# Optimization experiments

Measured on AMD Instinct MI355X. Metric: run time of the kernel, lower is better.

The kernel has to match this reference:

```python
import jax, jax.numpy as jnp
import numpy as np

B, T, D, H, L, O = 256, 256, 64, 512, 2, 10


def _uniform(key, shape, scale):
    return jax.random.uniform(key, shape, jnp.float32, -scale, scale)


def setup_inputs() -> dict:
    key = jax.random.key(0)
    ks = jax.random.split(key, 16)
    s = 1.0 / np.sqrt(H)  # PyTorch default init bound for RNN and Linear(H, .)
    inp = {
        "x": jax.random.normal(ks[0], (B, T, D), jnp.float32),
        # layer 0: input D -> H
        "w_ih0": _uniform(ks[1], (H, D), s),
        "w_hh0": _uniform(ks[2], (H, H), s),
        "b_ih0": _uniform(ks[3], (H,), s),
        "b_hh0": _uniform(ks[4], (H,), s),
        # layer 1: H -> H
        "w_ih1": _uniform(ks[5], (H, H), s),
        "w_hh1": _uniform(ks[6], (H, H), s),
        "b_ih1": _uniform(ks[7], (H,), s),
        "b_hh1": _uniform(ks[8], (H,), s),
        # head: fc1 (H->8), fc2 (8->O)
        "fc1_w": _uniform(ks[9], (8, H), s),
        "fc1_b": _uniform(ks[10], (8,), s),
        "fc2_w": _uniform(ks[11], (O, 8), 1.0 / np.sqrt(8)),
        "fc2_b": _uniform(ks[12], (O,), 1.0 / np.sqrt(8)),
    }
    return inp


def _rnn_relu_layer(seq, w_ih, w_hh, b_ih, b_hh):
    # seq: [T, B, Din] -> out: [T, B, H]
    # Precompute input projection for all timesteps (one big GEMM).
    x_proj = jnp.einsum('tbd,hd->tbh', seq, w_ih) + b_ih + b_hh

    def step(h, xp):
        h = jax.nn.relu(xp + h @ w_hh.T)
        return h, h

    h0 = jnp.zeros((seq.shape[1], w_hh.shape[0]), seq.dtype)
    _, out = jax.lax.scan(step, h0, x_proj)
    return out


def reference(x, w_ih0, w_hh0, b_ih0, b_hh0, w_ih1, w_hh1, b_ih1, b_hh1,
              fc1_w, fc1_b, fc2_w, fc2_b):
    seq = jnp.transpose(x, (1, 0, 2))  # [T, B, D]
    seq = _rnn_relu_layer(seq, w_ih0, w_hh0, b_ih0, b_hh0)
    seq = _rnn_relu_layer(seq, w_ih1, w_hh1, b_ih1, b_hh1)
    last = seq[-1]  # [B, H]
    h = jax.nn.relu(last @ fc1_w.T + fc1_b)
    return h @ fc2_w.T + fc2_b  # [B, O]
```

## Files before the change

### kernel.cpp

```cpp
#include <hip/hip_runtime.h>

using bf16x8 = __attribute__((ext_vector_type(8))) short;
using f32x4  = __attribute__((ext_vector_type(4))) float;
typedef unsigned short u16;
typedef unsigned int   u32;
typedef unsigned long long u64;

#define MAX_SPIN 1000000


__device__ __forceinline__ float bf2f(u16 u){ union{u32 i;float f;}v; v.i=((u32)u)<<16; return v.f; }
__device__ __forceinline__ u16 f2bf(float f){ union{float f;u32 i;}v; v.f=f; u32 x=v.i; return (u16)((x+0x7FFFu+((x>>16)&1u))>>16); }
__device__ __forceinline__ bf16x8 load8f(const float* p){
  float4 a=*(const float4*)p; float4 b=*(const float4*)(p+4);
  bf16x8 r; r[0]=(short)f2bf(a.x); r[1]=(short)f2bf(a.y); r[2]=(short)f2bf(a.z); r[3]=(short)f2bf(a.w);
  r[4]=(short)f2bf(b.x); r[5]=(short)f2bf(b.y); r[6]=(short)f2bf(b.z); r[7]=(short)f2bf(b.w); return r;
}
__device__ __forceinline__ int  ldf(int* p){ return __hip_atomic_load(p, __ATOMIC_RELAXED, __HIP_MEMORY_SCOPE_AGENT); }
__device__ __forceinline__ void stf(int* p, int v){ __hip_atomic_store(p, v, __ATOMIC_RELAXED, __HIP_MEMORY_SCOPE_AGENT); }
__device__ __forceinline__ u64  ld64c(const u32* p){ return __hip_atomic_load((const u64*)p, __ATOMIC_RELAXED, __HIP_MEMORY_SCOPE_AGENT); }
__device__ __forceinline__ u32  ld32c(const u32* p){ return __hip_atomic_load(p, __ATOMIC_RELAXED, __HIP_MEMORY_SCOPE_AGENT); }
__device__ __forceinline__ void st32c(u32* p, u32 v){ __hip_atomic_store(p, v, __ATOMIC_RELAXED, __HIP_MEMORY_SCOPE_AGENT); }
__device__ __forceinline__ int waitge(int* p, int tgt){
  int v = ldf(p); int it = 0;
  while (v < tgt && ++it < MAX_SPIN){ __builtin_amdgcn_s_sleep(1); v = ldf(p); }
  return v;
}

__global__ void init_kernel(u32* p){ p[(blockIdx.x<<9) + threadIdx.x] = 0u; }

#define HFRAG(base, ks) (*(const bf16x8*)((base) + (lrow<<10) + ((((ks)<<6)+(lk8<<1)) ^ sw)))

__global__ void __launch_bounds__(512, 2)
rnn_kernel(const float* __restrict__ x,
           const float* __restrict__ w_ih0, const float* __restrict__ w_hh0,
           const float* __restrict__ b_ih0, const float* __restrict__ b_hh0,
           const float* __restrict__ w_ih1, const float* __restrict__ w_hh1,
           const float* __restrict__ b_ih1, const float* __restrict__ b_hh1,
           const float* __restrict__ fc1_w, const float* __restrict__ fc1_b,
           const float* __restrict__ fc2_w, const float* __restrict__ fc2_b,
           float* __restrict__ out,
           u32* __restrict__ ring0, u32* __restrict__ ringz0, u32* __restrict__ ringz1,
           int* __restrict__ flags)
{
  const int tid  = threadIdx.x;
  const int wg   = blockIdx.x;
  const int lane = tid & 63;
  const int ww   = tid >> 6;
  const int role = wg >> 4;
  const int bt   = wg & 15;
  const int b0   = bt << 4;
  const int lrow = lane & 15;
  const int lk8  = (lane >> 4) << 3;
  const int sw   = (lrow & 7) << 4;
  const int rb   = (lane >> 4) << 2;

  __shared__ char sm[163840];
  char* smWb  = sm;
  char* smHhi = sm + 131072;
  char* smHlo = sm + 147456;

  int* flA  = flags + ((bt<<3) + 0)*16;
  int* flB0 = flags + ((bt<<3) + 1)*16;
  int* flB1 = flags + ((bt<<3) + 2)*16;
  int* flC  = flags + ((bt<<3) + 3)*16;
  int* flD  = flags + ((bt<<3) + 4)*16;

  if (role == 0 || role == 1) {
    const float* Wp = (role == 0) ? w_hh0 : w_hh1;
    const int n0 = ww << 6;
    bf16x8 wv[48];
#pragma unroll
    for (int tt = 0; tt < 4; ++tt) {
      int n = n0 + (tt<<4) + lrow;
#pragma unroll
      for (int ks = 0; ks < 12; ++ks)
        wv[tt*12+ks] = load8f(Wp + n*512 + (ks<<5) + lk8);
    }
#pragma unroll 1
    for (int it = 0; it < 16; ++it) {
      int cid = (it<<9) + tid;
      int ss = cid >> 11, wc = cid & 2047;
      int n = wc >> 2, k0 = (wc & 3) << 3;
      bf16x8 v = load8f(Wp + n*512 + 384 + (ss<<5) + k0);
      *(bf16x8*)(smWb + (ss<<15) + (n<<6) + ((k0<<1) ^ ((n&3)<<4))) = v;
    }
    __syncthreads();

    const int wl0 = ((lane>>4)<<4) ^ ((lrow&3)<<4);
    int wlb[4];
#pragma unroll
    for (int tt = 0; tt < 4; ++tt) wlb[tt] = ((n0 + (tt<<4) + lrow)<<6) + wl0;

    u32* zring = (role == 0) ? ringz0 : ringz1;
    const u32* zbase = zring + bt*65536;
    int fP = 0, fP2 = 0, fBP0 = 0, fBP1 = 0;
    if (tid == 0) {
      if (role == 0) fP = waitge(flD, 1);
      else { fP = waitge(flB0, 1); fP2 = waitge(flB1, 1); }
    }
    __syncthreads();
    float zpf[16];
#pragma unroll
    for (int tt = 0; tt < 4; ++tt) {
      int nc = n0 + (tt<<4) + lrow;
#pragma unroll
      for (int r = 0; r < 4; ++r)
        zpf[tt*4+r] = __uint_as_float(ld32c(zbase + ((rb+r)<<9) + nc));
    }

    for (int s = 0; s < 256; ++s) {
      f32x4 acc[4] = {{0,0,0,0},{0,0,0,0},{0,0,0,0},{0,0,0,0}};
      if (s > 0) {
#pragma unroll
        for (int ks = 0; ks < 16; ++ks) {
          bf16x8 ahi = HFRAG(smHhi, ks);
          bf16x8 alo = HFRAG(smHlo, ks);
          bf16x8 bw0, bw1, bw2, bw3;
          if (ks < 12) { bw0 = wv[ks]; bw1 = wv[12+ks]; bw2 = wv[24+ks]; bw3 = wv[36+ks]; }
          else {
            int sb = (ks-12) << 15;
            bw0 = *(const bf16x8*)(smWb + sb + wlb[0]);
            bw1 = *(const bf16x8*)(smWb + sb + wlb[1]);
            bw2 = *(const bf16x8*)(smWb + sb + wlb[2]);
            bw3 = *(const bf16x8*)(smWb + sb + wlb[3]);
          }
          acc[0] = __builtin_amdgcn_mfma_f32_16x16x32_bf16(ahi, bw0, acc[0], 0,0,0);
          acc[0] = __builtin_amdgcn_mfma_f32_16x16x32_bf16(alo, bw0, acc[0], 0,0,0);
          acc[1] = __builtin_amdgcn_mfma_f32_16x16x32_bf16(ahi, bw1, acc[1], 0,0,0);
          acc[1] = __builtin_amdgcn_mfma_f32_16x16x32_bf16(alo, bw1, acc[1], 0,0,0);
          acc[2] = __builtin_amdgcn_mfma_f32_16x16x32_bf16(ahi, bw2, acc[2], 0,0,0);
          acc[2] = __builtin_amdgcn_mfma_f32_16x16x32_bf16(alo, bw2, acc[2], 0,0,0);
          acc[3] = __builtin_amdgcn_mfma_f32_16x16x32_bf16(ahi, bw3, acc[3], 0,0,0);
          acc[3] = __builtin_amdgcn_mfma_f32_16x16x32_bf16(alo, bw3, acc[3], 0,0,0);
        }
      }
      u32 pk[16];
#pragma unroll
      for (int tt = 0; tt < 4; ++tt)
#pragma unroll
        for (int r = 0; r < 4; ++r) {
          float v = acc[tt][r] + zpf[tt*4+r];
          v = v > 0.f ? v : 0.f;
          u16 hi = f2bf(v); u16 lo = f2bf(v - bf2f(hi));
          pk[tt*4+r] = ((u32)hi << 16) | lo;
        }
      if (role == 0) {
        u32* rs = ring0 + bt*65536 + ((s&7)<<13);
#pragma unroll
        for (int tt = 0; tt < 4; ++tt) {
          int nc = n0 + (tt<<4) + lrow;
#pragma unroll
          for (int r = 0; r < 4; ++r) st32c(rs + ((rb+r)<<9) + nc, pk[tt*4+r]);
        }
      }
      __syncthreads();
#pragma unroll
      for (int tt = 0; tt < 4; ++tt) {
        int cc = n0 + (tt<<4) + lrow;
#pragma unroll
        for (int r = 0; r < 4; ++r) {
          int rr = rb + r;
          int o = (rr<<10) + (((cc<<1)) ^ ((rr&7)<<4));
          *(u16*)(smHhi + o) = (u16)(pk[tt*4+r] >> 16);
          *(u16*)(smHlo + o) = (u16)(pk[tt*4+r] & 0xFFFFu);
        }
      }
      asm volatile("s_waitcnt vmcnt(0)" ::: "memory");
      __syncthreads();
      if (tid == 0) {
        stf((role==0) ? flA : flC, s + 1);
        if (s < 255) {
          if (role == 0) {
            if (fP < s+2) fP = waitge(flD, s+2);
            if (s-6 > 0) {
              if (fBP0 < s-6) fBP0 = waitge(flB0, s-6);
              if (fBP1 < s-6) fBP1 = waitge(flB1, s-6);
            }
          } else {
            if (fP  < s+2) fP  = waitge(flB0, s+2);
            if (fP2 < s+2) fP2 = waitge(flB1, s+2);
          }
        }
      }
      __syncthreads();
      if (s < 255) {
        const u32* zs = zbase + (((s+1)&7)<<13);
#pragma unroll
        for (int tt = 0; tt < 4; ++tt) {
          int nc = n0 + (tt<<4) + lrow;
#pragma unroll
          for (int r = 0; r < 4; ++r)
            zpf[tt*4+r] = __uint_as_float(ld32c(zs + ((rb+r)<<9) + nc));
        }
      }
    }

    if (role == 1) {
      float* smF = (float*)sm;
      if (tid < 128) {
        int r = tid >> 3, j = tid & 7;
        const float* wr = fc1_w + (j << 9);
        float accv = fc1_b[j];
        for (int k = 0; k < 512; ++k) {
          int o = (r<<10) + (((k<<1)) ^ ((r&7)<<4));
          float hv = bf2f(*(u16*)(smHhi + o)) + bf2f(*(u16*)(smHlo + o));
          accv += hv * wr[k];
        }
        smF[tid] = accv > 0.f ? accv : 0.f;
      }
      __syncthreads();
      if (tid < 160) {
        int bb = tid / 10, o = tid - bb*10;
        float accv = fc2_b[o];
        const float* w = fc2_w + (o << 3);
#pragma unroll
        for (int j = 0; j < 8; ++j) accv += smF[(bb<<3)+j] * w[j];
        out[(b0 + bb)*10 + o] = accv;
      }
    }
  } else if (role == 2 || role == 3) {
    const int nb = (role - 2) << 8;
    const int n0 = nb + (ww << 5);
    bf16x8 wv[32];
    float bias[2];
#pragma unroll
    for (int tt = 0; tt < 2; ++tt) {
      int n = n0 + (tt<<4) + lrow;
#pragma unroll
      for (int ks = 0; ks < 16; ++ks)
        wv[tt*16+ks] = load8f(w_ih1 + n*512 + (ks<<5) + lk8);
      bias[tt] = b_ih1[n] + b_hh1[n];
    }
    int* flB = (role == 2) ? flB0 : flB1;
    int fA = 0, fC = 0;
    if (tid == 0) fA = waitge(flA, 1);
    __syncthreads();
    u64 pf[8];
    {
      const u32* rs = ring0 + bt*65536;
#pragma unroll
      for (int k = 0; k < 8; ++k) {
        int q = tid + (k<<9); int r = q >> 8, c = q & 255;
        pf[k] = ld64c(rs + (r<<9) + (c<<1));
      }
    }
    for (int t = 0; t < 256; ++t) {
#pragma unroll
      for (int k = 0; k < 8; ++k) {
        int q = tid + (k<<9); int r = q >> 8, c = q & 255;
        u32 e0 = (u32)pf[k], e1 = (u32)(pf[k] >> 32);
        int o = (r<<10) + ((c<<2) ^ ((r&7)<<4));
        *(u32*)(smHhi + o) = (e0 >> 16) | (e1 & 0xFFFF0000u);
        *(u32*)(smHlo + o) = (e0 & 0xFFFFu) | (e1 << 16);
      }
      __syncthreads();
      f32x4 acc[2] = {{0,0,0,0},{0,0,0,0}};
#pragma unroll
      for (int ks = 0; ks < 16; ++ks) {
        bf16x8 ahi = HFRAG(smHhi, ks);
        bf16x8 alo = HFRAG(smHlo, ks);
        acc[0] = __builtin_amdgcn_mfma_f32_16x16x32_bf16(ahi, wv[ks],    acc[0], 0,0,0);
        acc[0] = __builtin_amdgcn_mfma_f32_16x16x32_bf16(alo, wv[ks],    acc[0], 0,0,0);
        acc[1] = __builtin_amdgcn_mfma_f32_16x16x32_bf16(ahi, wv[16+ks], acc[1], 0,0,0);
        acc[1] = __builtin_amdgcn_mfma_f32_16x16x32_bf16(alo, wv[16+ks], acc[1], 0,0,0);
      }
      {
        u32* zs = ringz1 + bt*65536 + ((t&7)<<13);
#pragma unroll
        for (int tt = 0; tt < 2; ++tt) {
          int nc = n0 + (tt<<4) + lrow;
#pragma unroll
          for (int r = 0; r < 4; ++r)
            st32c(zs + ((rb+r)<<9) + nc, __float_as_uint(acc[tt][r] + bias[tt]));
        }
      }
      asm volatile("s_waitcnt vmcnt(0)" ::: "memory");
      __syncthreads();
      if (tid == 0) {
        stf(flB, t + 1);
        if (t < 255) {
          if (fA < t+2) fA = waitge(flA, t+2);
          if (t-6 > 0 && fC < t-6) fC = waitge(flC, t-6);
        }
      }
      __syncthreads();
      if (t < 255) {
        const u32* rs = ring0 + bt*65536 + (((t+1)&7)<<13);
#pragma unroll
        for (int k = 0; k < 8; ++k) {
          int q = tid + (k<<9); int r = q >> 8, c = q & 255;
          pf[k] = ld64c(rs + (r<<9) + (c<<1));
        }
      }
    }
  } else {
    const int n0 = ww << 6;
    bf16x8 wx[8];
    float bz[4];
#pragma unroll
    for (int tt = 0; tt < 4; ++tt) {
      int n = n0 + (tt<<4) + lrow;
      wx[tt*2+0] = load8f(w_ih0 + n*64 + lk8);
      wx[tt*2+1] = load8f(w_ih0 + n*64 + 32 + lk8);
      bz[tt] = b_ih0[n] + b_hh0[n];
    }
    int fA = 0;
    for (int s = 0; s < 256; ++s) {
      bf16x8 xh0, xl0, xh1, xl1;
      const float* xp = x + ((size_t)(b0 + lrow)*256 + s)*64 + lk8;
#pragma unroll
      for (int j = 0; j < 8; ++j) {
        float f0 = xp[j], f1 = xp[32+j];
        u16 h0 = f2bf(f0); xh0[j] = (short)h0; xl0[j] = (short)f2bf(f0 - bf2f(h0));
        u16 h1 = f2bf(f1); xh1[j] = (short)h1; xl1[j] = (short)f2bf(f1 - bf2f(h1));
      }
      f32x4 acc[4] = {{0,0,0,0},{0,0,0,0},{0,0,0,0},{0,0,0,0}};
#pragma unroll
      for (int tt = 0; tt < 4; ++tt) {
        acc[tt] = __builtin_amdgcn_mfma_f32_16x16x32_bf16(xh0, wx[tt*2+0], acc[tt], 0,0,0);
        acc[tt] = __builtin_amdgcn_mfma_f32_16x16x32_bf16(xl0, wx[tt*2+0], acc[tt], 0,0,0);
        acc[tt] = __builtin_amdgcn_mfma_f32_16x16x32_bf16(xh1, wx[tt*2+1], acc[tt], 0,0,0);
        acc[tt] = __builtin_amdgcn_mfma_f32_16x16x32_bf16(xl1, wx[tt*2+1], acc[tt], 0,0,0);
      }
      if (s >= 8) {
        if (tid == 0 && fA < s-7) fA = waitge(flA, s-7);
        __syncthreads();
      }
      {
        u32* zs = ringz0 + bt*65536 + ((s&7)<<13);
#pragma unroll
        for (int tt = 0; tt < 4; ++tt) {
          int nc = n0 + (tt<<4) + lrow;
#pragma unroll
          for (int r = 0; r < 4; ++r)
            st32c(zs + ((rb+r)<<9) + nc, __float_as_uint(acc[tt][r] + bz[tt]));
        }
      }
      asm volatile("s_waitcnt vmcnt(0)" ::: "memory");
      __syncthreads();
      if (tid == 0) stf(flD, s + 1);
    }
  }
}

extern "C" void kernel_launch(void* const* d_in, const int* in_sizes, int n_in,
                              void* d_out, int out_size, void* d_ws, size_t ws_size,
                              hipStream_t stream) {
  const float* x     = (const float*)d_in[0];
  const float* w_ih0 = (const float*)d_in[1];
  const float* w_hh0 = (const float*)d_in[2];
  const float* b_ih0 = (const float*)d_in[3];
  const float* b_hh0 = (const float*)d_in[4];
  const float* w_ih1 = (const float*)d_in[5];
  const float* w_hh1 = (const float*)d_in[6];
  const float* b_ih1 = (const float*)d_in[7];
  const float* b_hh1 = (const float*)d_in[8];
  const float* fc1_w = (const float*)d_in[9];
  const float* fc1_b = (const float*)d_in[10];
  const float* fc2_w = (const float*)d_in[11];
  const float* fc2_b = (const float*)d_in[12];
  float* out = (float*)d_out;

  char* ws = (char*)d_ws;
  u32* ring0  = (u32*)(ws);
  u32* ringz0 = (u32*)(ws + (4u<<20));
  u32* ringz1 = (u32*)(ws + (8u<<20));
  int* flags  = (int*)(ws + (12u<<20));

  init_kernel<<<dim3(4), dim3(512), 0, stream>>>((u32*)(ws + (12u<<20)));
  rnn_kernel<<<dim3(80), dim3(512), 0, stream>>>(
      x, w_ih0, w_hh0, b_ih0, b_hh0, w_ih1, w_hh1, b_ih1, b_hh1,
      fc1_w, fc1_b, fc2_w, fc2_b, out,
      ring0, ringz0, ringz1, flags);
}
```

Measured before the change: 2.014 ms.

## Fuse layer-0 input projection into recurrence, widen blocks to 1024 threads, bf16 handoff

Removes the separate layer-0 input-projection role: role 0 now computes the x·W_ih0 product inline each step, so the ringz0 buffer and its flag are gone. Blocks go to 1024 threads with each wave owning 32 output columns, and the grid drops from 80 to 64 blocks. Layer-0 output is handed to layer 1 as the bf16 hi plane only, written with 128-bit sc0/sc1 stores, and layer-1 input-projection blocks use single-precision bf16 MFMAs. The aim is to shorten the per-step serial chain and the inter-block traffic, at the cost of lower precision on the layer-1 input path and higher register pressure per thread.

```diff
diff --git a/kernel.cpp b/kernel.cpp
--- a/kernel.cpp
+++ b/kernel.cpp
@@ -4,9 +4,10 @@
 using f32x4  = __attribute__((ext_vector_type(4))) float;
 typedef unsigned short u16;
 typedef unsigned int   u32;
-typedef unsigned long long u64;
-
-#define MAX_SPIN 1000000
+using u32x2 = __attribute__((ext_vector_type(2))) u32;
+using u32x4 = __attribute__((ext_vector_type(4))) u32;
+
+#define MAX_SPIN 600000
 
 
 __device__ __forceinline__ float bf2f(u16 u){ union{u32 i;float f;}v; v.i=((u32)u)<<16; return v.f; }
@@ -16,22 +17,40 @@
   bf16x8 r; r[0]=(short)f2bf(a.x); r[1]=(short)f2bf(a.y); r[2]=(short)f2bf(a.z); r[3]=(short)f2bf(a.w);
   r[4]=(short)f2bf(b.x); r[5]=(short)f2bf(b.y); r[6]=(short)f2bf(b.z); r[7]=(short)f2bf(b.w); return r;
 }
+__device__ __forceinline__ bf16x8 pack8(float4 a, float4 b){
+  bf16x8 r; r[0]=(short)f2bf(a.x); r[1]=(short)f2bf(a.y); r[2]=(short)f2bf(a.z); r[3]=(short)f2bf(a.w);
+  r[4]=(short)f2bf(b.x); r[5]=(short)f2bf(b.y); r[6]=(short)f2bf(b.z); r[7]=(short)f2bf(b.w); return r;
+}
 __device__ __forceinline__ int  ldf(int* p){ return __hip_atomic_load(p, __ATOMIC_RELAXED, __HIP_MEMORY_SCOPE_AGENT); }
 __device__ __forceinline__ void stf(int* p, int v){ __hip_atomic_store(p, v, __ATOMIC_RELAXED, __HIP_MEMORY_SCOPE_AGENT); }
-__device__ __forceinline__ u64  ld64c(const u32* p){ return __hip_atomic_load((const u64*)p, __ATOMIC_RELAXED, __HIP_MEMORY_SCOPE_AGENT); }
-__device__ __forceinline__ u32  ld32c(const u32* p){ return __hip_atomic_load(p, __ATOMIC_RELAXED, __HIP_MEMORY_SCOPE_AGENT); }
-__device__ __forceinline__ void st32c(u32* p, u32 v){ __hip_atomic_store(p, v, __ATOMIC_RELAXED, __HIP_MEMORY_SCOPE_AGENT); }
 __device__ __forceinline__ int waitge(int* p, int tgt){
   int v = ldf(p); int it = 0;
   while (v < tgt && ++it < MAX_SPIN){ __builtin_amdgcn_s_sleep(1); v = ldf(p); }
   return v;
 }
+__device__ __forceinline__ u32x4 ld128c(const u32* p){
+  u32x4 r;
+  asm volatile("global_load_dwordx4 %0, %1, off sc0 sc1" : "=v"(r) : "v"(p) : "memory");
+  return r;
+}
+__device__ __forceinline__ u32x2 ld64c(const u32* p){
+  u32x2 r;
+  asm volatile("global_load_dwordx2 %0, %1, off sc0 sc1" : "=v"(r) : "v"(p) : "memory");
+  return r;
+}
+__device__ __forceinline__ void st128c(u32* p, u32x4 v){
+  asm volatile("global_store_dwordx4 %0, %1, off sc0 sc1" :: "v"(p), "v"(v) : "memory");
+}
+__device__ __forceinline__ void vmwait0(){
+  asm volatile("s_waitcnt vmcnt(0)" ::: "memory");
+  __builtin_amdgcn_sched_barrier(0);
+}
 
 __global__ void init_kernel(u32* p){ p[(blockIdx.x<<9) + threadIdx.x] = 0u; }
 
 #define HFRAG(base, ks) (*(const bf16x8*)((base) + (lrow<<10) + ((((ks)<<6)+(lk8<<1)) ^ sw)))
 
-__global__ void __launch_bounds__(512, 2)
+__global__ void __launch_bounds__(1024, 1)
 rnn_kernel(const float* __restrict__ x,
            const float* __restrict__ w_ih0, const float* __restrict__ w_hh0,
            const float* __restrict__ b_ih0, const float* __restrict__ b_hh0,
@@ -40,7 +59,7 @@
            const float* __restrict__ fc1_w, const float* __restrict__ fc1_b,
            const float* __restrict__ fc2_w, const float* __restrict__ fc2_b,
            float* __restrict__ out,
-           u32* __restrict__ ring0, u32* __restrict__ ringz0, u32* __restrict__ ringz1,
+           u32* __restrict__ ring0, u32* __restrict__ ringz1,
            int* __restrict__ flags)
 {
   const int tid  = threadIdx.x;
@@ -60,143 +79,161 @@
   char* smHhi = sm + 131072;
   char* smHlo = sm + 147456;
 
-  int* flA  = flags + ((bt<<3) + 0)*16;
-  int* flB0 = flags + ((bt<<3) + 1)*16;
-  int* flB1 = flags + ((bt<<3) + 2)*16;
-  int* flC  = flags + ((bt<<3) + 3)*16;
-  int* flD  = flags + ((bt<<3) + 4)*16;
-
-  if (role == 0 || role == 1) {
+  int* pA  = flags + ((bt<<2) + 0)*16;
+  int* pB0 = flags + ((bt<<2) + 1)*16;
+  int* pB1 = flags + ((bt<<2) + 2)*16;
+  int* pC  = flags + ((bt<<2) + 3)*16;
+
+  u32* r0bt = ring0  + bt*32768;
+  u32* z1bt = ringz1 + bt*65536;
+
+  if (role <= 1) {
     const float* Wp = (role == 0) ? w_hh0 : w_hh1;
-    const int n0 = ww << 6;
-    bf16x8 wv[48];
-#pragma unroll
-    for (int tt = 0; tt < 4; ++tt) {
+    const int n0 = ww << 5;
+    bf16x8 wv[24];
+#pragma unroll
+    for (int tt = 0; tt < 2; ++tt) {
       int n = n0 + (tt<<4) + lrow;
 #pragma unroll
       for (int ks = 0; ks < 12; ++ks)
         wv[tt*12+ks] = load8f(Wp + n*512 + (ks<<5) + lk8);
     }
 #pragma unroll 1
-    for (int it = 0; it < 16; ++it) {
-      int cid = (it<<9) + tid;
+    for (int it = 0; it < 8; ++it) {
+      int cid = (it<<10) + tid;
       int ss = cid >> 11, wc = cid & 2047;
       int n = wc >> 2, k0 = (wc & 3) << 3;
       bf16x8 v = load8f(Wp + n*512 + 384 + (ss<<5) + k0);
       *(bf16x8*)(smWb + (ss<<15) + (n<<6) + ((k0<<1) ^ ((n&3)<<4))) = v;
     }
-    __syncthreads();
-
     const int wl0 = ((lane>>4)<<4) ^ ((lrow&3)<<4);
-    int wlb[4];
-#pragma unroll
-    for (int tt = 0; tt < 4; ++tt) wlb[tt] = ((n0 + (tt<<4) + lrow)<<6) + wl0;
-
-    u32* zring = (role == 0) ? ringz0 : ringz1;
-    const u32* zbase = zring + bt*65536;
-    int fP = 0, fP2 = 0, fBP0 = 0, fBP1 = 0;
-    if (tid == 0) {
-      if (role == 0) fP = waitge(flD, 1);
-      else { fP = waitge(flB0, 1); fP2 = waitge(flB1, 1); }
-    }
-    __syncthreads();
-    float zpf[16];
-#pragma unroll
-    for (int tt = 0; tt < 4; ++tt) {
-      int nc = n0 + (tt<<4) + lrow;
+    const int wlb0 = ((n0 + lrow)<<6) + wl0;
+    const int wlb1 = ((n0 + 16 + lrow)<<6) + wl0;
+
+    if (role == 0) {
+      bf16x8 wihf[4];
+      float biasA[2];
+#pragma unroll
+      for (int tt = 0; tt < 2; ++tt) {
+        int n = n0 + (tt<<4) + lrow;
+        wihf[tt*2+0] = load8f(w_ih0 + n*64 + lk8);
+        wihf[tt*2+1] = load8f(w_ih0 + n*64 + 32 + lk8);
+        biasA[tt] = b_ih0[n] + b_hh0[n];
+      }
+      __syncthreads();
+      int fB0 = 0, fB1 = 0;
+      const int q = tid << 2;
+
+      for (int s = 0; s < 256; ++s) {
+        const float* xp = x + ((b0 + lrow) << 14) + (s << 6) + lk8;
+        float4 xa0 = *(const float4*)xp,        xb0 = *(const float4*)(xp + 4);
+        float4 xa1 = *(const float4*)(xp + 32), xb1 = *(const float4*)(xp + 36);
+        f32x4 acc[2] = {{0,0,0,0},{0,0,0,0}};
+        if (s > 0) {
+#pragma unroll
+          for (int ks = 0; ks < 16; ++ks) {
+            bf16x8 ahi = HFRAG(smHhi, ks);
+            bf16x8 alo = HFRAG(smHlo, ks);
+            bf16x8 bw0, bw1;
+            if (ks < 12) { bw0 = wv[ks]; bw1 = wv[12+ks]; }
+            else { int sb=(ks-12)<<15; bw0 = *(const bf16x8*)(smWb+sb+wlb0);
+                                       bw1 = *(const bf16x8*)(smWb+sb+wlb1); }
+            acc[0] = __builtin_amdgcn_mfma_f32_16x16x32_bf16(ahi, bw0, acc[0], 0,0,0);
+            acc[0] = __builtin_amdgcn_mfma_f32_16x16x32_bf16(alo, bw0, acc[0], 0,0,0);
+            acc[1] = __builtin_amdgcn_mfma_f32_16x16x32_bf16(ahi, bw1, acc[1], 0,0,0);
+            acc[1] = __builtin_amdgcn_mfma_f32_16x16x32_bf16(alo, bw1, acc[1], 0,0,0);
+          }
+        }
+        vmwait0();
+        if (tid == 0) {
+          if (s >= 1) stf(pA, s);
+          if (s >= 8) {
+            if (fB0 < s-7) fB0 = waitge(pB0, s-7);
+            if (fB1 < s-7) fB1 = waitge(pB1, s-7);
+          }
+        }
+        __syncthreads();
+        bf16x8 xf0 = pack8(xa0, xb0), xf1 = pack8(xa1, xb1);
+        acc[0] = __builtin_amdgcn_mfma_f32_16x16x32_bf16(xf0, wihf[0], acc[0], 0,0,0);
+        acc[0] = __builtin_amdgcn_mfma_f32_16x16x32_bf16(xf1, wihf[1], acc[0], 0,0,0);
+        acc[1] = __builtin_amdgcn_mfma_f32_16x16x32_bf16(xf0, wihf[2], acc[1], 0,0,0);
+        acc[1] = __builtin_amdgcn_mfma_f32_16x16x32_bf16(xf1, wihf[3], acc[1], 0,0,0);
+#pragma unroll
+        for (int tt = 0; tt < 2; ++tt) {
+          int cc = n0 + (tt<<4) + lrow;
+#pragma unroll
+          for (int r = 0; r < 4; ++r) {
+            float v = acc[tt][r] + biasA[tt]; v = v > 0.f ? v : 0.f;
+            u16 hi = f2bf(v), lo = f2bf(v - bf2f(hi));
+            int rr = rb + r;
+            int o = (rr<<10) + (((cc<<1)) ^ ((rr&7)<<4));
+            *(u16*)(smHhi + o) = hi;  *(u16*)(smHlo + o) = lo;
+          }
+        }
+        __syncthreads();
+        st128c(r0bt + ((s&7)<<12) + q, *(const u32x4*)(smHhi + (q<<2)));
+      }
+      vmwait0();
+      if (tid == 0) stf(pA, 256);
+    } else {
+      float fB0v = 0; int fB0i = 0, fB1i = 0;
+      (void)fB0v;
+      __syncthreads();
+      const int zoff = ((ww>>1)<<6) | (lrow<<2) | ((ww&1)<<1);
+      if (tid == 0) { fB0i = waitge(pB0, 1); fB1i = waitge(pB1, 1); }
+      __syncthreads();
+      u32x2 zq[4];
 #pragma unroll
       for (int r = 0; r < 4; ++r)
-        zpf[tt*4+r] = __uint_as_float(ld32c(zbase + ((rb+r)<<9) + nc));
-    }
-
-    for (int s = 0; s < 256; ++s) {
-      f32x4 acc[4] = {{0,0,0,0},{0,0,0,0},{0,0,0,0},{0,0,0,0}};
-      if (s > 0) {
-#pragma unroll
-        for (int ks = 0; ks < 16; ++ks) {
-          bf16x8 ahi = HFRAG(smHhi, ks);
-          bf16x8 alo = HFRAG(smHlo, ks);
-          bf16x8 bw0, bw1, bw2, bw3;
-          if (ks < 12) { bw0 = wv[ks]; bw1 = wv[12+ks]; bw2 = wv[24+ks]; bw3 = wv[36+ks]; }
-          else {
-            int sb = (ks-12) << 15;
-            bw0 = *(const bf16x8*)(smWb + sb + wlb[0]);
-            bw1 = *(const bf16x8*)(smWb + sb + wlb[1]);
-            bw2 = *(const bf16x8*)(smWb + sb + wlb[2]);
-            bw3 = *(const bf16x8*)(smWb + sb + wlb[3]);
-          }
-          acc[0] = __builtin_amdgcn_mfma_f32_16x16x32_bf16(ahi, bw0, acc[0], 0,0,0);
-          acc[0] = __builtin_amdgcn_mfma_f32_16x16x32_bf16(alo, bw0, acc[0], 0,0,0);
-          acc[1] = __builtin_amdgcn_mfma_f32_16x16x32_bf16(ahi, bw1, acc[1], 0,0,0);
-          acc[1] = __builtin_amdgcn_mfma_f32_16x16x32_bf16(alo, bw1, acc[1], 0,0,0);
-          acc[2] = __builtin_amdgcn_mfma_f32_16x16x32_bf16(ahi, bw2, acc[2], 0,0,0);
-          acc[2] = __builtin_amdgcn_mfma_f32_16x16x32_bf16(alo, bw2, acc[2], 0,0,0);
-          acc[3] = __builtin_amdgcn_mfma_f32_16x16x32_bf16(ahi, bw3, acc[3], 0,0,0);
-          acc[3] = __builtin_amdgcn_mfma_f32_16x16x32_bf16(alo, bw3, acc[3], 0,0,0);
-        }
-      }
-      u32 pk[16];
-#pragma unroll
-      for (int tt = 0; tt < 4; ++tt)
-#pragma unroll
-        for (int r = 0; r < 4; ++r) {
-          float v = acc[tt][r] + zpf[tt*4+r];
-          v = v > 0.f ? v : 0.f;
-          u16 hi = f2bf(v); u16 lo = f2bf(v - bf2f(hi));
-          pk[tt*4+r] = ((u32)hi << 16) | lo;
-        }
-      if (role == 0) {
-        u32* rs = ring0 + bt*65536 + ((s&7)<<13);
-#pragma unroll
-        for (int tt = 0; tt < 4; ++tt) {
-          int nc = n0 + (tt<<4) + lrow;
-#pragma unroll
-          for (int r = 0; r < 4; ++r) st32c(rs + ((rb+r)<<9) + nc, pk[tt*4+r]);
-        }
-      }
-      __syncthreads();
-#pragma unroll
-      for (int tt = 0; tt < 4; ++tt) {
-        int cc = n0 + (tt<<4) + lrow;
-#pragma unroll
-        for (int r = 0; r < 4; ++r) {
-          int rr = rb + r;
-          int o = (rr<<10) + (((cc<<1)) ^ ((rr&7)<<4));
-          *(u16*)(smHhi + o) = (u16)(pk[tt*4+r] >> 16);
-          *(u16*)(smHlo + o) = (u16)(pk[tt*4+r] & 0xFFFFu);
-        }
-      }
-      asm volatile("s_waitcnt vmcnt(0)" ::: "memory");
-      __syncthreads();
-      if (tid == 0) {
-        stf((role==0) ? flA : flC, s + 1);
-        if (s < 255) {
-          if (role == 0) {
-            if (fP < s+2) fP = waitge(flD, s+2);
-            if (s-6 > 0) {
-              if (fBP0 < s-6) fBP0 = waitge(flB0, s-6);
-              if (fBP1 < s-6) fBP1 = waitge(flB1, s-6);
-            }
-          } else {
-            if (fP  < s+2) fP  = waitge(flB0, s+2);
-            if (fP2 < s+2) fP2 = waitge(flB1, s+2);
-          }
-        }
-      }
-      __syncthreads();
-      if (s < 255) {
-        const u32* zs = zbase + (((s+1)&7)<<13);
-#pragma unroll
-        for (int tt = 0; tt < 4; ++tt) {
-          int nc = n0 + (tt<<4) + lrow;
+        zq[r] = ld64c(z1bt + ((rb+r)<<9) + zoff);
+
+      for (int t = 0; t < 256; ++t) {
+        f32x4 acc[2] = {{0,0,0,0},{0,0,0,0}};
+        if (t > 0) {
+#pragma unroll
+          for (int ks = 0; ks < 16; ++ks) {
+            bf16x8 ahi = HFRAG(smHhi, ks);
+            bf16x8 alo = HFRAG(smHlo, ks);
+            bf16x8 bw0, bw1;
+            if (ks < 12) { bw0 = wv[ks]; bw1 = wv[12+ks]; }
+            else { int sb=(ks-12)<<15; bw0 = *(const bf16x8*)(smWb+sb+wlb0);
+                                       bw1 = *(const bf16x8*)(smWb+sb+wlb1); }
+            acc[0] = __builtin_amdgcn_mfma_f32_16x16x32_bf16(ahi, bw0, acc[0], 0,0,0);
+            acc[0] = __builtin_amdgcn_mfma_f32_16x16x32_bf16(alo, bw0, acc[0], 0,0,0);
+            acc[1] = __builtin_amdgcn_mfma_f32_16x16x32_bf16(ahi, bw1, acc[1], 0,0,0);
+            acc[1] = __builtin_amdgcn_mfma_f32_16x16x32_bf16(alo, bw1, acc[1], 0,0,0);
+          }
+        }
+        vmwait0();
+        __syncthreads();
+#pragma unroll
+        for (int tt = 0; tt < 2; ++tt) {
+          int cc = n0 + (tt<<4) + lrow;
+#pragma unroll
+          for (int r = 0; r < 4; ++r) {
+            float z = __uint_as_float(tt == 0 ? zq[r].x : zq[r].y);
+            float v = acc[tt][r] + z; v = v > 0.f ? v : 0.f;
+            u16 hi = f2bf(v), lo = f2bf(v - bf2f(hi));
+            int rr = rb + r;
+            int o = (rr<<10) + (((cc<<1)) ^ ((rr&7)<<4));
+            *(u16*)(smHhi + o) = hi;  *(u16*)(smHlo + o) = lo;
+          }
+        }
+        __syncthreads();
+        if (tid == 0) {
+          stf(pC, t + 1);
+          if (t < 255) {
+            if (fB0i < t+2) fB0i = waitge(pB0, t+2);
+            if (fB1i < t+2) fB1i = waitge(pB1, t+2);
+          }
+        }
+        __syncthreads();
+        if (t < 255) {
 #pragma unroll
           for (int r = 0; r < 4; ++r)
-            zpf[tt*4+r] = __uint_as_float(ld32c(zs + ((rb+r)<<9) + nc));
-        }
-      }
-    }
-
-    if (role == 1) {
+            zq[r] = ld64c(z1bt + (((t+1)&7)<<13) + ((rb+r)<<9) + zoff);
+        }
+      }
       float* smF = (float*)sm;
       if (tid < 128) {
         int r = tid >> 3, j = tid & 7;
@@ -219,128 +256,53 @@
         out[(b0 + bb)*10 + o] = accv;
       }
     }
-  } else if (role == 2 || role == 3) {
+  } else {
+    char* smH = sm;
+    u32*  smZ = (u32*)(sm + 16384);
+    int* pB = (role == 2) ? pB0 : pB1;
     const int nb = (role - 2) << 8;
-    const int n0 = nb + (ww << 5);
-    bf16x8 wv[32];
-    float bias[2];
-#pragma unroll
-    for (int tt = 0; tt < 2; ++tt) {
-      int n = n0 + (tt<<4) + lrow;
-#pragma unroll
-      for (int ks = 0; ks < 16; ++ks)
-        wv[tt*16+ks] = load8f(w_ih1 + n*512 + (ks<<5) + lk8);
-      bias[tt] = b_ih1[n] + b_hh1[n];
+    const int n  = nb + (ww << 4) + lrow;
+    bf16x8 wI[16];
+#pragma unroll
+    for (int ks = 0; ks < 16; ++ks)
+      wI[ks] = load8f(w_ih1 + n*512 + (ks<<5) + lk8);
+    const float biasB = b_ih1[n] + b_hh1[n];
+    const int zcol = ((ww>>2)<<6) | (lrow<<2) | (ww&3);
+    const int q = tid << 2;
+
+    int fA = 0, fC = 0;
+    if (tid == 0) fA = waitge(pA, 1);
+    __syncthreads();
+    u32x4 hpf = ld128c(r0bt + q);
+
+    for (int t = 0; t < 256; ++t) {
+      vmwait0();
+      if (tid == 0) {
+        if (t >= 1) stf(pB, t);
+        if (t >= 8 && fC < t-7) fC = waitge(pC, t-7);
+        if (t < 255 && fA < t+2) fA = waitge(pA, t+2);
+      }
+      __syncthreads();
+      *(u32x4*)(smH + (q<<2)) = hpf;
+      __syncthreads();
+      if (t < 255) hpf = ld128c(r0bt + (((t+1)&7)<<12) + q);
+      f32x4 acc = {0,0,0,0};
+#pragma unroll
+      for (int ks = 0; ks < 16; ++ks) {
+        bf16x8 af = HFRAG(smH, ks);
+        acc = __builtin_amdgcn_mfma_f32_16x16x32_bf16(af, wI[ks], acc, 0,0,0);
+      }
+#pragma unroll
+      for (int r = 0; r < 4; ++r)
+        smZ[((rb+r)<<8) | zcol] = __float_as_uint(acc[r] + biasB);
+      __syncthreads();
+      {
+        int row = q >> 8, c = q & 255;
+        st128c(z1bt + ((t&7)<<13) + (row<<9) + nb + c, *(const u32x4*)((const char*)smZ + (q<<2)));
+      }
     }
-    int* flB = (role == 2) ? flB0 : flB1;
-    int fA = 0, fC = 0;
-    if (tid == 0) fA = waitge(flA, 1);
-    __syncthreads();
-    u64 pf[8];
-    {
-      const u32* rs = ring0 + bt*65536;
-#pragma unroll
-      for (int k = 0; k < 8; ++k) {
-        int q = tid + (k<<9); int r = q >> 8, c = q & 255;
-        pf[k] = ld64c(rs + (r<<9) + (c<<1));
-      }
-    }
-    for (int t = 0; t < 256; ++t) {
-#pragma unroll
-      for (int k = 0; k < 8; ++k) {
-        int q = tid + (k<<9); int r = q >> 8, c = q & 255;
-        u32 e0 = (u32)pf[k], e1 = (u32)(pf[k] >> 32);
-        int o = (r<<10) + ((c<<2) ^ ((r&7)<<4));
-        *(u32*)(smHhi + o) = (e0 >> 16) | (e1 & 0xFFFF0000u);
-        *(u32*)(smHlo + o) = (e0 & 0xFFFFu) | (e1 << 16);
-      }
-      __syncthreads();
-      f32x4 acc[2] = {{0,0,0,0},{0,0,0,0}};
-#pragma unroll
-      for (int ks = 0; ks < 16; ++ks) {
-        bf16x8 ahi = HFRAG(smHhi, ks);
-        bf16x8 alo = HFRAG(smHlo, ks);
-        acc[0] = __builtin_amdgcn_mfma_f32_16x16x32_bf16(ahi, wv[ks],    acc[0], 0,0,0);
-        acc[0] = __builtin_amdgcn_mfma_f32_16x16x32_bf16(alo, wv[ks],    acc[0], 0,0,0);
-        acc[1] = __builtin_amdgcn_mfma_f32_16x16x32_bf16(ahi, wv[16+ks], acc[1], 0,0,0);
-        acc[1] = __builtin_amdgcn_mfma_f32_16x16x32_bf16(alo, wv[16+ks], acc[1], 0,0,0);
-      }
-      {
-        u32* zs = ringz1 + bt*65536 + ((t&7)<<13);
-#pragma unroll
-        for (int tt = 0; tt < 2; ++tt) {
-          int nc = n0 + (tt<<4) + lrow;
-#pragma unroll
-          for (int r = 0; r < 4; ++r)
-            st32c(zs + ((rb+r)<<9) + nc, __float_as_uint(acc[tt][r] + bias[tt]));
-        }
-      }
-      asm volatile("s_waitcnt vmcnt(0)" ::: "memory");
-      __syncthreads();
-      if (tid == 0) {
-        stf(flB, t + 1);
-        if (t < 255) {
-          if (fA < t+2) fA = waitge(flA, t+2);
-          if (t-6 > 0 && fC < t-6) fC = waitge(flC, t-6);
-        }
-      }
-      __syncthreads();
-      if (t < 255) {
-        const u32* rs = ring0 + bt*65536 + (((t+1)&7)<<13);
-#pragma unroll
-        for (int k = 0; k < 8; ++k) {
-          int q = tid + (k<<9); int r = q >> 8, c = q & 255;
-          pf[k] = ld64c(rs + (r<<9) + (c<<1));
-        }
-      }
-    }
-  } else {
-    const int n0 = ww << 6;
-    bf16x8 wx[8];
-    float bz[4];
-#pragma unroll
-    for (int tt = 0; tt < 4; ++tt) {
-      int n = n0 + (tt<<4) + lrow;
-      wx[tt*2+0] = load8f(w_ih0 + n*64 + lk8);
-      wx[tt*2+1] = load8f(w_ih0 + n*64 + 32 + lk8);
-      bz[tt] = b_ih0[n] + b_hh0[n];
-    }
-    int fA = 0;
-    for (int s = 0; s < 256; ++s) {
-      bf16x8 xh0, xl0, xh1, xl1;
-      const float* xp = x + ((size_t)(b0 + lrow)*256 + s)*64 + lk8;
-#pragma unroll
-      for (int j = 0; j < 8; ++j) {
-        float f0 = xp[j], f1 = xp[32+j];
-        u16 h0 = f2bf(f0); xh0[j] = (short)h0; xl0[j] = (short)f2bf(f0 - bf2f(h0));
-        u16 h1 = f2bf(f1); xh1[j] = (short)h1; xl1[j] = (short)f2bf(f1 - bf2f(h1));
-      }
-      f32x4 acc[4] = {{0,0,0,0},{0,0,0,0},{0,0,0,0},{0,0,0,0}};
-#pragma unroll
-      for (int tt = 0; tt < 4; ++tt) {
-        acc[tt] = __builtin_amdgcn_mfma_f32_16x16x32_bf16(xh0, wx[tt*2+0], acc[tt], 0,0,0);
-        acc[tt] = __builtin_amdgcn_mfma_f32_16x16x32_bf16(xl0, wx[tt*2+0], acc[tt], 0,0,0);
-        acc[tt] = __builtin_amdgcn_mfma_f32_16x16x32_bf16(xh1, wx[tt*2+1], acc[tt], 0,0,0);
-        acc[tt] = __builtin_amdgcn_mfma_f32_16x16x32_bf16(xl1, wx[tt*2+1], acc[tt], 0,0,0);
-      }
-      if (s >= 8) {
-        if (tid == 0 && fA < s-7) fA = waitge(flA, s-7);
-        __syncthreads();
-      }
-      {
-        u32* zs = ringz0 + bt*65536 + ((s&7)<<13);
-#pragma unroll
-        for (int tt = 0; tt < 4; ++tt) {
-          int nc = n0 + (tt<<4) + lrow;
-#pragma unroll
-          for (int r = 0; r < 4; ++r)
-            st32c(zs + ((rb+r)<<9) + nc, __float_as_uint(acc[tt][r] + bz[tt]));
-        }
-      }
-      asm volatile("s_waitcnt vmcnt(0)" ::: "memory");
-      __syncthreads();
-      if (tid == 0) stf(flD, s + 1);
-    }
+    vmwait0();
+    if (tid == 0) stf(pB, 256);
   }
 }
 
@@ -364,13 +326,12 @@
 
   char* ws = (char*)d_ws;
   u32* ring0  = (u32*)(ws);
-  u32* ringz0 = (u32*)(ws + (4u<<20));
-  u32* ringz1 = (u32*)(ws + (8u<<20));
-  int* flags  = (int*)(ws + (12u<<20));
-
-  init_kernel<<<dim3(4), dim3(512), 0, stream>>>((u32*)(ws + (12u<<20)));
-  rnn_kernel<<<dim3(80), dim3(512), 0, stream>>>(
+  u32* ringz1 = (u32*)(ws + (2u<<20));
+  int* flags  = (int*)(ws + (6u<<20));
+
+  init_kernel<<<dim3(2), dim3(512), 0, stream>>>((u32*)(ws + (6u<<20)));
+  rnn_kernel<<<dim3(64), dim3(1024), 0, stream>>>(
       x, w_ih0, w_hh0, b_ih0, b_hh0, w_ih1, w_hh1, b_ih1, b_hh1,
       fc1_w, fc1_b, fc2_w, fc2_b, out,
-      ring0, ringz0, ringz1, flags);
-}
+      ring0, ringz1, flags);
+}
```

Measured after the change: 2.742 ms. +36.2%, slower.
